# Performance work log

Measured on AMD Instinct MI355X. Metric: run time of the kernel, lower is better.

Reference implementation:

```python
import jax, jax.numpy as jnp
import numpy as np

B, R, A, V, L = 256, 512, 196, 10000, 2
I = R  # input_size == rnn_size (required for stacked layers)


def setup_inputs() -> dict:
    key = jax.random.key(0)
    ks = jax.random.split(key, 18)
    s = 0.05
    return {
        "x": jax.random.normal(ks[0], (B, I), jnp.float32),
        "att": jax.random.normal(ks[1], (B, A, R), jnp.float32),
        "inputs": jax.random.normal(ks[2], (2 * L, B, R), jnp.float32),
        "Wa2a": jax.random.normal(ks[3], (A, R), jnp.float32) * s,
        "ba2a": jnp.zeros((A,), jnp.float32),
        "Wh2a": jax.random.normal(ks[4], (A, R), jnp.float32) * s,
        "bh2a": jnp.zeros((A,), jnp.float32),
        "wd2d": jax.random.normal(ks[5], (A,), jnp.float32) * s,
        "bd2d": jnp.zeros((1,), jnp.float32),
        "Wi2h": jax.random.normal(ks[6], (4 * R, I), jnp.float32) * s,
        "bi2h": jnp.zeros((4 * R,), jnp.float32),
        "Wh2h": jax.random.normal(ks[7], (4 * R, R), jnp.float32) * s,
        "bh2h": jnp.zeros((4 * R,), jnp.float32),
        "Wr2a": jax.random.normal(ks[8], (4 * R, R), jnp.float32) * s,
        "br2a": jnp.zeros((4 * R,), jnp.float32),
        "Wproj": jax.random.normal(ks[9], (V, R), jnp.float32) * s,
        "bproj": jnp.zeros((V,), jnp.float32),
    }


def reference(x, att, inputs, Wa2a, ba2a, Wh2a, bh2a, wd2d, bd2d,
              Wi2h, bi2h, Wh2h, bh2h, Wr2a, br2a, Wproj, bproj):
    # att: [B, A, R]  (A spatial positions, R features); inputs: [2L, B, R]
    states = []
    cur = x
    # a2a(att) is layer-independent but the original recomputes it; einsum below
    # is cheap so we keep the per-layer structure faithful & simple.
    for i in range(L):
        prev_c = inputs[2 * i]
        prev_h = inputs[2 * i + 1]
        # attention scoring: att_v[b,i,a] + att_h[b,i] (unsqueeze(2).expand)
        att_v = jnp.einsum('bir,ar->bia', att, Wa2a) + ba2a          # [B,A,A]
        att_h = prev_h @ Wh2a.T + bh2a                               # [B,A]
        dot = jnp.tanh(att_v + att_h[:, :, None])                    # [B,A,A]
        score = jnp.einsum('bia,a->bi', dot, wd2d) + bd2d            # [B,A]
        w = jax.nn.softmax(score, axis=-1)                           # [B,A]
        att_res = jnp.einsum('bir,bi->br', att, w)                   # [B,R]
        sums = (cur @ Wi2h.T + bi2h) + (prev_h @ Wh2h.T + bh2h) + (att_res @ Wr2a.T + br2a)
        gates = jax.nn.sigmoid(sums[:, :3 * R])
        in_gate = gates[:, :R]
        forget_gate = gates[:, R:2 * R]
        out_gate = gates[:, 2 * R:3 * R]
        in_transform = jnp.tanh(sums[:, 3 * R:])
        next_c = forget_gate * prev_c + in_gate * in_transform
        next_h = out_gate * jnp.tanh(next_c)
        states.append(next_c)
        states.append(next_h)
        cur = next_h
    logsoft = jax.nn.log_softmax(cur @ Wproj.T + bproj, axis=-1)     # [B,V]
    return jnp.stack(states), logsoft
```

## Files before the change

### kernel.cpp

```cpp
#include <hip/hip_runtime.h>
#include <hip/hip_bf16.h>
#include <cstdint>
#include <cstddef>

#define BB 256
#define RR 512
#define AA 196
#define VV 10000
#define MATT (BB*AA)
#define NT13 13

typedef float f32x4 __attribute__((ext_vector_type(4)));
typedef __bf16 bf16x8 __attribute__((ext_vector_type(8)));
typedef __bf16 bf16x4 __attribute__((ext_vector_type(4)));

#define MFMA16(a,b,c) __builtin_amdgcn_mfma_f32_16x16x32_bf16(a,b,c,0,0,0)

__device__ __forceinline__ float fast_tanh(float x){
  float ax = fabsf(x);
  float e = __expf(-2.0f*ax);
  float t = __fdividef(1.0f - e, 1.0f + e);
  return x < 0.0f ? -t : t;
}

__device__ __forceinline__ void gload16(const void* gsrc, void* ldsdst){
  __builtin_amdgcn_global_load_lds(
      (const __attribute__((address_space(1))) unsigned int*)gsrc,
      (__attribute__((address_space(3))) unsigned int*)ldsdst,
      16, 0, 0);
}

#define ABAR   asm volatile("s_barrier" ::: "memory")
#define WVM(N) asm volatile("s_waitcnt vmcnt(" #N ")" ::: "memory")

#define CVT8(a, f0, f1) do { \
  a[0]=(__bf16)(f0).x; a[1]=(__bf16)(f0).y; a[2]=(__bf16)(f0).z; a[3]=(__bf16)(f0).w; \
  a[4]=(__bf16)(f1).x; a[5]=(__bf16)(f1).y; a[6]=(__bf16)(f1).z; a[7]=(__bf16)(f1).w; \
} while(0)

__global__ void prep_all_k(
    const float* __restrict__ Wa2a, const float* __restrict__ Wh2a,
    const float* __restrict__ Wproj, const float* __restrict__ inputs,
    const float* __restrict__ Wi2h, const float* __restrict__ Wh2h,
    const float* __restrict__ Wr2a, const float* __restrict__ ba2a,
    const float* __restrict__ wd2d, const float* __restrict__ bi2h,
    const float* __restrict__ bh2h, const float* __restrict__ br2a,
    __bf16* __restrict__ Wa2a_p, __bf16* __restrict__ Wh2a_pad,
    __bf16* __restrict__ Wproj_bf, __bf16* __restrict__ inp_bf,
    __bf16* __restrict__ Wcat_bf,
    float* __restrict__ ba_pad, float* __restrict__ wd_pad, float* __restrict__ bcat)
{
  size_t q = (size_t)blockIdx.x*256 + threadIdx.x;
  float4 v = {0,0,0,0};
  __bf16* dst = nullptr;
  size_t dq = 0;
  if (q < 32768){
    int row = q >> 7, k4 = q & 127;
    if (row < AA) v = ((const float4*)(Wa2a + (size_t)row*512))[k4];
    dst = Wa2a_p; dq = q;
  } else if (q < 65536){
    size_t ql = q - 32768;
    int row = ql >> 7, k4 = ql & 127;
    if (row < AA) v = ((const float4*)(Wh2a + (size_t)row*512))[k4];
    dst = Wh2a_pad; dq = ql;
  } else if (q < 1351680){
    size_t ql = q - 65536;
    int row = ql >> 7, k4 = ql & 127;
    if (row < VV) v = ((const float4*)(Wproj + (size_t)row*512))[k4];
    dst = Wproj_bf; dq = ql;
  } else if (q < 1417216){
    size_t ql = q - 1351680;
    const float* src = (ql < 32768) ? (inputs + 1*131072) : (inputs + 3*131072 - 131072);
    v = ((const float4*)src)[ql];
    dst = inp_bf; dq = ql;
  } else if (q < 2203648){
    size_t ql = q - 1417216;
    int n = ql / 384, k4 = ql - (size_t)n*384;
    if (k4 < 128)      v = ((const float4*)(Wi2h + (size_t)n*512))[k4];
    else if (k4 < 256) v = ((const float4*)(Wh2h + (size_t)n*512))[k4-128];
    else               v = ((const float4*)(Wr2a + (size_t)n*512))[k4-256];
    dst = Wcat_bf; dq = (size_t)n*384 + k4;
  } else {
    size_t i = q - 2203648;
    if (i < 2048)       bcat[i] = bi2h[i] + bh2h[i] + br2a[i];
    else if (i < 2304){ int j = i - 2048; ba_pad[j] = (j < AA) ? ba2a[j] : 0.0f; }
    else              { int j = i - 2304; wd_pad[j] = (j < AA) ? wd2d[j] : 0.0f; }
    return;
  }
  bf16x4 o;
  o[0]=(__bf16)v.x; o[1]=(__bf16)v.y; o[2]=(__bf16)v.z; o[3]=(__bf16)v.w;
  ((bf16x4*)dst)[dq] = o;
}

__global__ __launch_bounds__(256,4) void gemm3_k(
    const __bf16* __restrict__ A, const __bf16* __restrict__ Bw,
    const float* __restrict__ bias, float* __restrict__ C,
    int N, int K, int NC)
{
  __shared__ __bf16 AshAll[3*2048];
  __shared__ __bf16 BshAll[3*4096];
  const int t = threadIdx.x;
  const int l = t & 63;
  const int w = t >> 6;
  const int l15 = l & 15;
  const int g  = l >> 4;
  const int rho = l15 & 7;
  const int mrow = blockIdx.y*32;
  const int ncb  = blockIdx.x*64;

  const int arow = t >> 3, aj = t & 7;
  const __bf16* as_ = A + (size_t)(mrow + arow)*K + ((aj ^ (arow&7)) << 3);
  const int aoff = w*512;
  const __bf16* bs0_ = Bw + (size_t)(ncb + arow)*K      + ((aj ^ (arow&7)) << 3);
  const __bf16* bs1_ = Bw + (size_t)(ncb + 32 + arow)*K + ((aj ^ (arow&7)) << 3);
  const int boff0 = w*512;
  const int boff1 = 2048 + w*512;

#define G3_STAGE(B, CH) do { \
    gload16(as_  + (CH)*64, AshAll + (B)*2048 + aoff); \
    gload16(bs0_ + (CH)*64, BshAll + (B)*4096 + boff0); \
    gload16(bs1_ + (CH)*64, BshAll + (B)*4096 + boff1); \
  } while(0)

  f32x4 acc0 = {}, acc1 = {};

#define G3_COMPUTE(B) do { \
    const __bf16* As_ = AshAll + (B)*2048; \
    const __bf16* Bs_ = BshAll + (B)*4096; \
    _Pragma("unroll") \
    for (int s_ = 0; s_ < 2; s_++){ \
      int q_ = (((s_<<2)+g) ^ rho) << 3; \
      bf16x8 a0_ = *(const bf16x8*)(As_ + l15*64 + q_); \
      bf16x8 a1_ = *(const bf16x8*)(As_ + (l15+16)*64 + q_); \
      bf16x8 b_  = *(const bf16x8*)(Bs_ + (w*16+l15)*64 + q_); \
      acc0 = MFMA16(a0_, b_, acc0); \
      acc1 = MFMA16(a1_, b_, acc1); \
    } \
  } while(0)

  G3_STAGE(0,0); G3_STAGE(1,1); G3_STAGE(2,2);
  WVM(6); ABAR;
  int buf = 0;
  for (int c = 0; c < NC; c++){
    G3_COMPUTE(buf);
    if (c + 3 < NC){
      ABAR;
      G3_STAGE(buf, c+3);
      WVM(6); ABAR;
    } else if (c == NC-3){
      WVM(3); ABAR;
    } else if (c == NC-2){
      WVM(0); ABAR;
    }
    buf = (buf == 2) ? 0 : buf + 1;
  }

  int col = ncb + w*16 + l15;
  if (col < N){
    float bv = bias[col];
    #pragma unroll
    for (int r = 0; r < 4; r++){
      C[(size_t)(mrow + g*4 + r)*N + col]      = acc0[r] + bv;
      C[(size_t)(mrow + 16 + g*4 + r)*N + col] = acc1[r] + bv;
    }
  }
#undef G3_STAGE
#undef G3_COMPUTE
}

__global__ __launch_bounds__(256,3) void att_score9_k(
    const float* __restrict__ att, const __bf16* __restrict__ Wa2a_p,
    const float* __restrict__ ba_pad, const float* __restrict__ wd_pad,
    const float* __restrict__ att_h, float* __restrict__ score)
{
  __shared__ float  Ash[2*2048];
  __shared__ __bf16 Bsh[2*6656];
  const int t = threadIdx.x;
  const int l = t & 63;
  const int w = t >> 6;
  const int l15 = l & 15, g = l >> 4;
  const int bid = blockIdx.x;
  const int tile = (bid & 7) * 98 + (bid >> 3);
  const int rowbase = tile * 64;

  const float* aSrc[2]; int aoff[2];
  #pragma unroll
  for (int i = 0; i < 2; i++){
    int slot = i*256 + t;
    int row = slot >> 3, sub = slot & 7;
    aoff[i] = (i*256 + w*64) * 4;
    aSrc[i] = att + (size_t)(rowbase + row)*RR + ((sub ^ (row&7)) << 2);
  }
  const __bf16* bSrc[4]; int boff[4];
  #pragma unroll
  for (int i = 0; i < 4; i++){
    int slot = (i < 3) ? (i*256 + t) : (768 + l);
    int row = slot >> 2, j = slot & 3;
    boff[i] = ((i < 3) ? (i*256 + w*64) : 768) * 8;
    bSrc[i] = Wa2a_p + (size_t)row*RR + ((j ^ (row&3)) << 3);
  }

  f32x4 acc[NT13] = {};

#define S9_STAGE(BUF, CH) do { \
    const int kc_ = (CH)*32; \
    gload16(aSrc[0] + kc_, Ash + (BUF)*2048 + aoff[0]); \
    gload16(aSrc[1] + kc_, Ash + (BUF)*2048 + aoff[1]); \
    gload16(bSrc[0] + kc_, Bsh + (BUF)*6656 + boff[0]); \
    gload16(bSrc[1] + kc_, Bsh + (BUF)*6656 + boff[1]); \
    gload16(bSrc[2] + kc_, Bsh + (BUF)*6656 + boff[2]); \
    gload16(bSrc[3] + kc_, Bsh + (BUF)*6656 + boff[3]); \
  } while(0)

  const int arow = w*16 + l15;
  const int ao0 = arow*32 + (((2*g)   ^ (arow&7)) << 2);
  const int ao1 = arow*32 + (((2*g+1) ^ (arow&7)) << 2);

#define S9_COMPUTE(BUF) do { \
    const float*  As_ = Ash + (BUF)*2048; \
    const __bf16* Bs_ = Bsh + (BUF)*6656; \
    float4 fa0 = *(const float4*)(As_ + ao0); \
    float4 fa1 = *(const float4*)(As_ + ao1); \
    bf16x8 a_; CVT8(a_, fa0, fa1); \
    _Pragma("unroll") \
    for (int nt_ = 0; nt_ < NT13; nt_++){ \
      int br_ = nt_*16 + l15; \
      bf16x8 b_ = *(const bf16x8*)(Bs_ + br_*32 + ((g ^ (br_&3)) << 3)); \
      acc[nt_] = MFMA16(a_, b_, acc[nt_]); \
    } \
  } while(0)

  S9_STAGE(0,0); S9_STAGE(1,1); WVM(6);
  ABAR;
  #pragma unroll
  for (int c = 0; c < 16; c++){
    S9_COMPUTE(c & 1);
    if (c < 14){
      ABAR;
      S9_STAGE(c & 1, c + 2);
      WVM(6);
      ABAR;
    } else if (c == 14){
      WVM(0);
      ABAR;
    }
  }

  float wdv[NT13], bav[NT13];
  #pragma unroll
  for (int nt = 0; nt < NT13; nt++){
    int col = nt*16 + l15;
    wdv[nt] = wd_pad[col];
    bav[nt] = ba_pad[col];
  }
  #pragma unroll
  for (int r = 0; r < 4; r++){
    int row = rowbase + w*16 + g*4 + r;
    float ah0 = att_h[row];
    float ah1 = att_h[MATT + row];
    float s0 = 0.0f, s1 = 0.0f;
    #pragma unroll
    for (int nt = 0; nt < NT13; nt++){
      float v = acc[nt][r] + bav[nt];
      s0 += fast_tanh(v + ah0) * wdv[nt];
      s1 += fast_tanh(v + ah1) * wdv[nt];
    }
    #pragma unroll
    for (int o = 1; o < 16; o <<= 1){
      s0 += __shfl_xor(s0, o, 16);
      s1 += __shfl_xor(s1, o, 16);
    }
    if (l15 == 0){
      score[row] = s0;
      score[MATT + row] = s1;
    }
  }
#undef S9_STAGE
#undef S9_COMPUTE
}

__global__ __launch_bounds__(512) void attres_sm_k(
    const float* __restrict__ att, const float* __restrict__ score,
    const float* __restrict__ x, const float* __restrict__ inputs,
    __bf16* __restrict__ Xcat0, __bf16* __restrict__ Xcat1)
{
  int b = blockIdx.x, t = threadIdx.x;
  __shared__ float wv[2][256];
  __shared__ float4 redv[4][128];
  const int w = t >> 6, l = t & 63;

  if (w < 2){
    const float* s = score + (size_t)w*MATT + (size_t)b*AA;
    float v[4], e[4];
    #pragma unroll
    for (int j = 0; j < 4; j++){
      int i = l + j*64;
      v[j] = (i < AA) ? s[i] : -3.4e38f;
    }
    float mx = fmaxf(fmaxf(v[0],v[1]), fmaxf(v[2],v[3]));
    #pragma unroll
    for (int o = 1; o < 64; o <<= 1) mx = fmaxf(mx, __shfl_xor(mx, o, 64));
    float sum = 0.0f;
    #pragma unroll
    for (int j = 0; j < 4; j++){
      int i = l + j*64;
      e[j] = (i < AA) ? __expf(v[j] - mx) : 0.0f;
      sum += e[j];
    }
    #pragma unroll
    for (int o = 1; o < 64; o <<= 1) sum += __shfl_xor(sum, o, 64);
    float inv = 1.0f / sum;
    #pragma unroll
    for (int j = 0; j < 4; j++) wv[w][l + j*64] = e[j]*inv;
  }
  Xcat0[(size_t)b*1536 + t]       = (__bf16)x[(size_t)b*512 + t];
  Xcat0[(size_t)b*1536 + 512 + t] = (__bf16)inputs[(size_t)1*131072 + b*512 + t];
  Xcat1[(size_t)b*1536 + 512 + t] = (__bf16)inputs[(size_t)3*131072 + b*512 + t];
  __syncthreads();

  int cg = t & 127, ig = t >> 7;
  const float4* ap = (const float4*)(att + (size_t)b*AA*RR) + cg;
  float4 s0 = {0,0,0,0}, s1 = {0,0,0,0};
  #pragma unroll 4
  for (int i = ig; i < AA; i += 4){
    float4 v = ap[(size_t)i*128];
    float a0 = wv[0][i], a1 = wv[1][i];
    s0.x += v.x*a0; s0.y += v.y*a0; s0.z += v.z*a0; s0.w += v.w*a0;
    s1.x += v.x*a1; s1.y += v.y*a1; s1.z += v.z*a1; s1.w += v.w*a1;
  }
  redv[ig][cg] = s0; __syncthreads();
  if (t < 128){
    float4 a = redv[0][t], b4 = redv[1][t], c4 = redv[2][t], d4 = redv[3][t];
    bf16x4 o;
    o[0]=(__bf16)(a.x+b4.x+c4.x+d4.x); o[1]=(__bf16)(a.y+b4.y+c4.y+d4.y);
    o[2]=(__bf16)(a.z+b4.z+c4.z+d4.z); o[3]=(__bf16)(a.w+b4.w+c4.w+d4.w);
    *(bf16x4*)(Xcat0 + (size_t)b*1536 + 1024 + t*4) = o;
  }
  __syncthreads();
  redv[ig][cg] = s1; __syncthreads();
  if (t < 128){
    float4 a = redv[0][t], b4 = redv[1][t], c4 = redv[2][t], d4 = redv[3][t];
    bf16x4 o;
    o[0]=(__bf16)(a.x+b4.x+c4.x+d4.x); o[1]=(__bf16)(a.y+b4.y+c4.y+d4.y);
    o[2]=(__bf16)(a.z+b4.z+c4.z+d4.z); o[3]=(__bf16)(a.w+b4.w+c4.w+d4.w);
    *(bf16x4*)(Xcat1 + (size_t)b*1536 + 1024 + t*4) = o;
  }
}

__global__ void gate_k(const float* __restrict__ sums, const float* __restrict__ prev_c,
                       float* __restrict__ out_c, float* __restrict__ out_h,
                       __bf16* __restrict__ hdst, int hstride){
  int idx = blockIdx.x*256 + threadIdx.x;
  int b = idx >> 9, r = idx & 511;
  const float* s = sums + (size_t)b*2048;
  float ig = 1.0f/(1.0f + __expf(-s[r]));
  float fg = 1.0f/(1.0f + __expf(-s[512+r]));
  float og = 1.0f/(1.0f + __expf(-s[1024+r]));
  float g  = fast_tanh(s[1536+r]);
  float c = fg*prev_c[idx] + ig*g;
  float h = og*fast_tanh(c);
  out_c[idx] = c;
  out_h[idx] = h;
  hdst[(size_t)b*hstride + r] = (__bf16)h;
}

__global__ void logsoftmax4_k(const float* __restrict__ logits, float* __restrict__ out){
  int b = blockIdx.x, t = threadIdx.x;
  __shared__ float red[4], red2[4];
  const float4* p = (const float4*)(logits + (size_t)b*VV);
  float mx = -3.4e38f;
  for (int i = t; i < 2500; i += 256){
    float4 v = p[i];
    mx = fmaxf(mx, fmaxf(fmaxf(v.x,v.y), fmaxf(v.z,v.w)));
  }
  #pragma unroll
  for (int o = 1; o < 64; o <<= 1) mx = fmaxf(mx, __shfl_xor(mx, o, 64));
  if ((t & 63) == 0) red[t >> 6] = mx;
  __syncthreads();
  mx = fmaxf(fmaxf(red[0], red[1]), fmaxf(red[2], red[3]));
  float sum = 0.0f;
  for (int i = t; i < 2500; i += 256){
    float4 v = p[i];
    sum += __expf(v.x-mx) + __expf(v.y-mx) + __expf(v.z-mx) + __expf(v.w-mx);
  }
  #pragma unroll
  for (int o = 1; o < 64; o <<= 1) sum += __shfl_xor(sum, o, 64);
  if ((t & 63) == 0) red2[t >> 6] = sum;
  __syncthreads();
  sum = red2[0] + red2[1] + red2[2] + red2[3];
  float lse = mx + logf(sum);
  float4* q = (float4*)(out + (size_t)b*VV);
  for (int i = t; i < 2500; i += 256){
    float4 v = p[i];
    v.x -= lse; v.y -= lse; v.z -= lse; v.w -= lse;
    q[i] = v;
  }
}

extern "C" void kernel_launch(void* const* d_in, const int* in_sizes, int n_in,
                              void* d_out_, int out_size, void* d_ws, size_t ws_size,
                              hipStream_t stream){
  const float* x     = (const float*)d_in[0];
  const float* att   = (const float*)d_in[1];
  const float* inputs= (const float*)d_in[2];
  const float* Wa2a  = (const float*)d_in[3];
  const float* ba2a  = (const float*)d_in[4];
  const float* Wh2a  = (const float*)d_in[5];
  const float* bh2a  = (const float*)d_in[6];
  const float* wd2d  = (const float*)d_in[7];
  const float* Wi2h  = (const float*)d_in[9];
  const float* bi2h  = (const float*)d_in[10];
  const float* Wh2h  = (const float*)d_in[11];
  const float* bh2h  = (const float*)d_in[12];
  const float* Wr2a  = (const float*)d_in[13];
  const float* br2a  = (const float*)d_in[14];
  const float* Wproj = (const float*)d_in[15];
  const float* bproj = (const float*)d_in[16];
  float* d_out = (float*)d_out_;

  char* wsp = (char*)d_ws;
  auto alloc = [&](size_t bytes)->char*{
    char* p = wsp;
    wsp += (bytes + 255) & ~(size_t)255;
    return p;
  };
  __bf16* Wa2a_p   = (__bf16*)alloc((size_t)256*RR*2);
  __bf16* Wh2a_pad = (__bf16*)alloc((size_t)256*RR*2);
  __bf16* Wcat_bf  = (__bf16*)alloc((size_t)2048*1536*2);
  __bf16* Wproj_bf = (__bf16*)alloc((size_t)10048*RR*2);
  __bf16* inp_bf   = (__bf16*)alloc((size_t)512*RR*2);
  float* ba_pad = (float*)alloc(256*4);
  float* wd_pad = (float*)alloc(256*4);
  float* bcat   = (float*)alloc(2048*4);
  float* att_h  = (float*)alloc((size_t)2*MATT*4);
  float* score  = (float*)alloc((size_t)2*MATT*4);
  __bf16* Xcat0 = (__bf16*)alloc((size_t)BB*1536*2);
  __bf16* Xcat1 = (__bf16*)alloc((size_t)BB*1536*2);
  float* sums   = (float*)alloc((size_t)BB*2048*4);
  __bf16* h1_bf = (__bf16*)alloc((size_t)BB*RR*2);
  float* logits = (float*)alloc((size_t)BB*VV*4);

  prep_all_k<<<8618, 256, 0, stream>>>(
      Wa2a, Wh2a, Wproj, inputs, Wi2h, Wh2h, Wr2a, ba2a, wd2d, bi2h, bh2h, br2a,
      Wa2a_p, Wh2a_pad, Wproj_bf, inp_bf, Wcat_bf, ba_pad, wd_pad, bcat);

  gemm3_k<<<dim3(4,16), 256, 0, stream>>>(inp_bf, Wh2a_pad, bh2a, att_h, AA, 512, 8);

  att_score9_k<<<784, 256, 0, stream>>>(att, Wa2a_p, ba_pad, wd_pad, att_h, score);
  attres_sm_k<<<256, 512, 0, stream>>>(att, score, x, inputs, Xcat0, Xcat1);

  gemm3_k<<<dim3(32,8), 256, 0, stream>>>(Xcat0, Wcat_bf, bcat, sums, 2048, 1536, 24);
  gate_k<<<512, 256, 0, stream>>>(sums, inputs, d_out, d_out + 131072, Xcat1, 1536);
  gemm3_k<<<dim3(32,8), 256, 0, stream>>>(Xcat1, Wcat_bf, bcat, sums, 2048, 1536, 24);
  gate_k<<<512, 256, 0, stream>>>(sums, inputs + 2*131072, d_out + 2*131072, d_out + 3*131072, h1_bf, 512);

  gemm3_k<<<dim3(157,8), 256, 0, stream>>>(h1_bf, Wproj_bf, bproj, logits, VV, 512, 8);
  logsoftmax4_k<<<256, 256, 0, stream>>>(logits, d_out + 4*131072);
}
```

Measured before the change: 139.4 us.

## Enlarge attention-score tile to 256 rows with triple-buffered staging

The attention scoring kernel now processes 256 rows of att per block instead of 64, so each wave computes four 16-row fragments against each loaded Wa2a tile. The Wa2a B-tile is therefore reused four times per load, and staging moves to a three-deep buffer with padded rows (stride 36). The grid shrinks from 784 to 196 blocks at occupancy 1, which trades latency hiding and CU coverage (196 blocks on a 256-CU part) for fewer redundant weight loads. Accumulator register use grows fourfold.

```diff
diff --git a/kernel.cpp b/kernel.cpp
--- a/kernel.cpp
+++ b/kernel.cpp
@@ -168,28 +168,28 @@
 #undef G3_COMPUTE
 }
 
-__global__ __launch_bounds__(256,3) void att_score9_k(
+__global__ __launch_bounds__(256,1) void att_score10_k(
     const float* __restrict__ att, const __bf16* __restrict__ Wa2a_p,
     const float* __restrict__ ba_pad, const float* __restrict__ wd_pad,
     const float* __restrict__ att_h, float* __restrict__ score)
 {
-  __shared__ float  Ash[2*2048];
-  __shared__ __bf16 Bsh[2*6656];
+  __shared__ float  Ash[3*9216];
+  __shared__ __bf16 Bsh[3*6656];
   const int t = threadIdx.x;
   const int l = t & 63;
   const int w = t >> 6;
   const int l15 = l & 15, g = l >> 4;
-  const int bid = blockIdx.x;
-  const int tile = (bid & 7) * 98 + (bid >> 3);
-  const int rowbase = tile * 64;
-
-  const float* aSrc[2]; int aoff[2];
-  #pragma unroll
-  for (int i = 0; i < 2; i++){
+  const int rowbase = blockIdx.x * 256;
+
+  const float* aSrc[9]; int aoff[9];
+  #pragma unroll
+  for (int i = 0; i < 9; i++){
     int slot = i*256 + t;
-    int row = slot >> 3, sub = slot & 7;
+    int row = slot / 9;
+    int sub = slot - row*9;
+    int subx = (sub < 8) ? (sub ^ (row&7)) : (0 ^ (row&7));
     aoff[i] = (i*256 + w*64) * 4;
-    aSrc[i] = att + (size_t)(rowbase + row)*RR + ((sub ^ (row&7)) << 2);
+    aSrc[i] = att + (size_t)(rowbase + row)*RR + (subx << 2);
   }
   const __bf16* bSrc[4]; int boff[4];
   #pragma unroll
@@ -200,49 +200,50 @@
     bSrc[i] = Wa2a_p + (size_t)row*RR + ((j ^ (row&3)) << 3);
   }
 
-  f32x4 acc[NT13] = {};
-
-#define S9_STAGE(BUF, CH) do { \
+  f32x4 acc[4][NT13] = {};
+
+#define S10_STAGE(BUF, CH) do { \
     const int kc_ = (CH)*32; \
-    gload16(aSrc[0] + kc_, Ash + (BUF)*2048 + aoff[0]); \
-    gload16(aSrc[1] + kc_, Ash + (BUF)*2048 + aoff[1]); \
-    gload16(bSrc[0] + kc_, Bsh + (BUF)*6656 + boff[0]); \
-    gload16(bSrc[1] + kc_, Bsh + (BUF)*6656 + boff[1]); \
-    gload16(bSrc[2] + kc_, Bsh + (BUF)*6656 + boff[2]); \
-    gload16(bSrc[3] + kc_, Bsh + (BUF)*6656 + boff[3]); \
+    _Pragma("unroll") \
+    for (int i_ = 0; i_ < 9; i_++) gload16(aSrc[i_] + kc_, Ash + (BUF)*9216 + aoff[i_]); \
+    _Pragma("unroll") \
+    for (int i_ = 0; i_ < 4; i_++) gload16(bSrc[i_] + kc_, Bsh + (BUF)*6656 + boff[i_]); \
   } while(0)
 
-  const int arow = w*16 + l15;
-  const int ao0 = arow*32 + (((2*g)   ^ (arow&7)) << 2);
-  const int ao1 = arow*32 + (((2*g+1) ^ (arow&7)) << 2);
-
-#define S9_COMPUTE(BUF) do { \
-    const float*  As_ = Ash + (BUF)*2048; \
+#define S10_COMPUTE(BUF) do { \
+    const float*  As_ = Ash + (BUF)*9216; \
     const __bf16* Bs_ = Bsh + (BUF)*6656; \
-    float4 fa0 = *(const float4*)(As_ + ao0); \
-    float4 fa1 = *(const float4*)(As_ + ao1); \
-    bf16x8 a_; CVT8(a_, fa0, fa1); \
+    bf16x8 afr[4]; \
+    _Pragma("unroll") \
+    for (int f_ = 0; f_ < 4; f_++){ \
+      int ar_ = w*64 + f_*16 + l15; \
+      float4 fa0 = *(const float4*)(As_ + ar_*36 + (((2*g)   ^ (ar_&7)) << 2)); \
+      float4 fa1 = *(const float4*)(As_ + ar_*36 + (((2*g+1) ^ (ar_&7)) << 2)); \
+      CVT8(afr[f_], fa0, fa1); \
+    } \
     _Pragma("unroll") \
     for (int nt_ = 0; nt_ < NT13; nt_++){ \
       int br_ = nt_*16 + l15; \
       bf16x8 b_ = *(const bf16x8*)(Bs_ + br_*32 + ((g ^ (br_&3)) << 3)); \
-      acc[nt_] = MFMA16(a_, b_, acc[nt_]); \
+      _Pragma("unroll") \
+      for (int f_ = 0; f_ < 4; f_++) acc[f_][nt_] = MFMA16(afr[f_], b_, acc[f_][nt_]); \
     } \
   } while(0)
 
-  S9_STAGE(0,0); S9_STAGE(1,1); WVM(6);
-  ABAR;
+  S10_STAGE(0,0); S10_STAGE(1,1); S10_STAGE(2,2);
+  WVM(26); ABAR;
   #pragma unroll
   for (int c = 0; c < 16; c++){
-    S9_COMPUTE(c & 1);
-    if (c < 14){
+    S10_COMPUTE(c % 3);
+    if (c < 13){
       ABAR;
-      S9_STAGE(c & 1, c + 2);
-      WVM(6);
+      S10_STAGE(c % 3, c + 3);
+      WVM(26);
       ABAR;
+    } else if (c == 13){
+      WVM(13); ABAR;
     } else if (c == 14){
-      WVM(0);
-      ABAR;
+      WVM(0); ABAR;
     }
   }
 
@@ -254,29 +255,32 @@
     bav[nt] = ba_pad[col];
   }
   #pragma unroll
-  for (int r = 0; r < 4; r++){
-    int row = rowbase + w*16 + g*4 + r;
-    float ah0 = att_h[row];
-    float ah1 = att_h[MATT + row];
-    float s0 = 0.0f, s1 = 0.0f;
-    #pragma unroll
-    for (int nt = 0; nt < NT13; nt++){
-      float v = acc[nt][r] + bav[nt];
-      s0 += fast_tanh(v + ah0) * wdv[nt];
-      s1 += fast_tanh(v + ah1) * wdv[nt];
-    }
-    #pragma unroll
-    for (int o = 1; o < 16; o <<= 1){
-      s0 += __shfl_xor(s0, o, 16);
-      s1 += __shfl_xor(s1, o, 16);
-    }
-    if (l15 == 0){
-      score[row] = s0;
-      score[MATT + row] = s1;
-    }
-  }
-#undef S9_STAGE
-#undef S9_COMPUTE
+  for (int f = 0; f < 4; f++){
+    #pragma unroll
+    for (int r = 0; r < 4; r++){
+      int row = rowbase + w*64 + f*16 + g*4 + r;
+      float ah0 = att_h[row];
+      float ah1 = att_h[MATT + row];
+      float s0 = 0.0f, s1 = 0.0f;
+      #pragma unroll
+      for (int nt = 0; nt < NT13; nt++){
+        float v = acc[f][nt][r] + bav[nt];
+        s0 += fast_tanh(v + ah0) * wdv[nt];
+        s1 += fast_tanh(v + ah1) * wdv[nt];
+      }
+      #pragma unroll
+      for (int o = 1; o < 16; o <<= 1){
+        s0 += __shfl_xor(s0, o, 16);
+        s1 += __shfl_xor(s1, o, 16);
+      }
+      if (l15 == 0){
+        score[row] = s0;
+        score[MATT + row] = s1;
+      }
+    }
+  }
+#undef S10_STAGE
+#undef S10_COMPUTE
 }
 
 __global__ __launch_bounds__(512) void attres_sm_k(
@@ -446,7 +450,7 @@
 
   gemm3_k<<<dim3(4,16), 256, 0, stream>>>(inp_bf, Wh2a_pad, bh2a, att_h, AA, 512, 8);
 
-  att_score9_k<<<784, 256, 0, stream>>>(att, Wa2a_p, ba_pad, wd_pad, att_h, score);
+  att_score10_k<<<196, 256, 0, stream>>>(att, Wa2a_p, ba_pad, wd_pad, att_h, score);
   attres_sm_k<<<256, 512, 0, stream>>>(att, score, x, inputs, Xcat0, Xcat1);
 
   gemm3_k<<<dim3(32,8), 256, 0, stream>>>(Xcat0, Wcat_bf, bcat, sums, 2048, 1536, 24);
```

Result: slower. 146.0 us (+4.8%).

## Load attention-score MFMA operands directly from global memory, dropping LDS staging

Applied to the files above, without the earlier changes.

The attention scoring kernel no longer double-buffers att and Wa2a tiles through shared memory with barriers. Each lane now reads its A fragment and all 13 B fragments straight from global memory, relying on L1/L2 caching of the small Wa2a matrix. Occupancy hint rises from 3 to 4 blocks. This removes the LDS traffic and synchronisation, but every wave refetches the B weights from cache, and global loads are no longer overlapped with compute through explicit prefetch.

```diff
diff --git a/kernel.cpp b/kernel.cpp
--- a/kernel.cpp
+++ b/kernel.cpp
@@ -168,13 +168,11 @@
 #undef G3_COMPUTE
 }
 
-__global__ __launch_bounds__(256,3) void att_score9_k(
+__global__ __launch_bounds__(256,4) void att_score11_k(
     const float* __restrict__ att, const __bf16* __restrict__ Wa2a_p,
     const float* __restrict__ ba_pad, const float* __restrict__ wd_pad,
     const float* __restrict__ att_h, float* __restrict__ score)
 {
-  __shared__ float  Ash[2*2048];
-  __shared__ __bf16 Bsh[2*6656];
   const int t = threadIdx.x;
   const int l = t & 63;
   const int w = t >> 6;
@@ -182,67 +180,22 @@
   const int bid = blockIdx.x;
   const int tile = (bid & 7) * 98 + (bid >> 3);
   const int rowbase = tile * 64;
-
-  const float* aSrc[2]; int aoff[2];
-  #pragma unroll
-  for (int i = 0; i < 2; i++){
-    int slot = i*256 + t;
-    int row = slot >> 3, sub = slot & 7;
-    aoff[i] = (i*256 + w*64) * 4;
-    aSrc[i] = att + (size_t)(rowbase + row)*RR + ((sub ^ (row&7)) << 2);
-  }
-  const __bf16* bSrc[4]; int boff[4];
-  #pragma unroll
-  for (int i = 0; i < 4; i++){
-    int slot = (i < 3) ? (i*256 + t) : (768 + l);
-    int row = slot >> 2, j = slot & 3;
-    boff[i] = ((i < 3) ? (i*256 + w*64) : 768) * 8;
-    bSrc[i] = Wa2a_p + (size_t)row*RR + ((j ^ (row&3)) << 3);
-  }
+  const int row = rowbase + w*16 + l15;
+
+  const float*  pa = att + (size_t)row*RR + g*8;
+  const __bf16* pb = Wa2a_p + (size_t)l15*RR + g*8;
 
   f32x4 acc[NT13] = {};
-
-#define S9_STAGE(BUF, CH) do { \
-    const int kc_ = (CH)*32; \
-    gload16(aSrc[0] + kc_, Ash + (BUF)*2048 + aoff[0]); \
-    gload16(aSrc[1] + kc_, Ash + (BUF)*2048 + aoff[1]); \
-    gload16(bSrc[0] + kc_, Bsh + (BUF)*6656 + boff[0]); \
-    gload16(bSrc[1] + kc_, Bsh + (BUF)*6656 + boff[1]); \
-    gload16(bSrc[2] + kc_, Bsh + (BUF)*6656 + boff[2]); \
-    gload16(bSrc[3] + kc_, Bsh + (BUF)*6656 + boff[3]); \
-  } while(0)
-
-  const int arow = w*16 + l15;
-  const int ao0 = arow*32 + (((2*g)   ^ (arow&7)) << 2);
-  const int ao1 = arow*32 + (((2*g+1) ^ (arow&7)) << 2);
-
-#define S9_COMPUTE(BUF) do { \
-    const float*  As_ = Ash + (BUF)*2048; \
-    const __bf16* Bs_ = Bsh + (BUF)*6656; \
-    float4 fa0 = *(const float4*)(As_ + ao0); \
-    float4 fa1 = *(const float4*)(As_ + ao1); \
-    bf16x8 a_; CVT8(a_, fa0, fa1); \
-    _Pragma("unroll") \
-    for (int nt_ = 0; nt_ < NT13; nt_++){ \
-      int br_ = nt_*16 + l15; \
-      bf16x8 b_ = *(const bf16x8*)(Bs_ + br_*32 + ((g ^ (br_&3)) << 3)); \
-      acc[nt_] = MFMA16(a_, b_, acc[nt_]); \
-    } \
-  } while(0)
-
-  S9_STAGE(0,0); S9_STAGE(1,1); WVM(6);
-  ABAR;
-  #pragma unroll
+  #pragma unroll 2
   for (int c = 0; c < 16; c++){
-    S9_COMPUTE(c & 1);
-    if (c < 14){
-      ABAR;
-      S9_STAGE(c & 1, c + 2);
-      WVM(6);
-      ABAR;
-    } else if (c == 14){
-      WVM(0);
-      ABAR;
+    const int kc = c*32;
+    float4 f0 = *(const float4*)(pa + kc);
+    float4 f1 = *(const float4*)(pa + kc + 4);
+    bf16x8 a; CVT8(a, f0, f1);
+    #pragma unroll
+    for (int nt = 0; nt < NT13; nt++){
+      bf16x8 b = *(const bf16x8*)(pb + (size_t)nt*16*RR + kc);
+      acc[nt] = MFMA16(a, b, acc[nt]);
     }
   }
 
@@ -255,9 +208,9 @@
   }
   #pragma unroll
   for (int r = 0; r < 4; r++){
-    int row = rowbase + w*16 + g*4 + r;
-    float ah0 = att_h[row];
-    float ah1 = att_h[MATT + row];
+    int orow = rowbase + w*16 + g*4 + r;
+    float ah0 = att_h[orow];
+    float ah1 = att_h[MATT + orow];
     float s0 = 0.0f, s1 = 0.0f;
     #pragma unroll
     for (int nt = 0; nt < NT13; nt++){
@@ -271,12 +224,10 @@
       s1 += __shfl_xor(s1, o, 16);
     }
     if (l15 == 0){
-      score[row] = s0;
-      score[MATT + row] = s1;
-    }
-  }
-#undef S9_STAGE
-#undef S9_COMPUTE
+      score[orow] = s0;
+      score[MATT + orow] = s1;
+    }
+  }
 }
 
 __global__ __launch_bounds__(512) void attres_sm_k(
@@ -446,7 +397,7 @@
 
   gemm3_k<<<dim3(4,16), 256, 0, stream>>>(inp_bf, Wh2a_pad, bh2a, att_h, AA, 512, 8);
 
-  att_score9_k<<<784, 256, 0, stream>>>(att, Wa2a_p, ba_pad, wd_pad, att_h, score);
+  att_score11_k<<<784, 256, 0, stream>>>(att, Wa2a_p, ba_pad, wd_pad, att_h, score);
   attres_sm_k<<<256, 512, 0, stream>>>(att, score, x, inputs, Xcat0, Xcat1);
 
   gemm3_k<<<dim3(32,8), 256, 0, stream>>>(Xcat0, Wcat_bf, bcat, sums, 2048, 1536, 24);
```

New measurement: 214.7 us. +54.0%, slower.
